# Performance work log

Hardware: AMD Instinct MI355X
Metric: run time of the kernel (lower is better)

## Reference

```python
import jax, jax.numpy as jnp
import numpy as np

# hyperparameters (see init_kwargs)
DP, DS, DO, D, K, C = 256, 256, 64, 320, 10, 10
SI, NS = 100, 22
ALIGN = 0.05
COEF = 0.3989422917366028  # 1/sqrt(2*pi)
B, SEQ, T_STEPS = 32, 512, 200


def _linear_params(key, fan_in, fan_out):
    # torch nn.Linear default init: U(-1/sqrt(fan_in), 1/sqrt(fan_in))
    s = 1.0 / np.sqrt(fan_in)
    kw, kb = jax.random.split(key)
    w = jax.random.uniform(kw, (fan_in, fan_out), minval=-s, maxval=s, dtype=jnp.float32)
    b = jax.random.uniform(kb, (fan_out,), minval=-s, maxval=s, dtype=jnp.float32)
    return w, b


def setup_inputs() -> dict:
    key = jax.random.key(0)
    ks = jax.random.split(key, 8)
    sentence = jax.random.randint(ks[0], (B, SEQ), 0, SI)
    speaker_id = jax.random.randint(ks[1], (B,), 0, NS)
    Lut_P = jax.random.normal(ks[2], (SI, DP), dtype=jnp.float32)
    Lut_S = jax.random.normal(ks[3], (NS, DS), dtype=jnp.float32)
    Na_w, Na_b = _linear_params(ks[4], D * K, 3 * C)
    Nu_w, Nu_b = _linear_params(ks[5], D * K, D)
    No_w, No_b = _linear_params(ks[6], D * K, DO)
    kf = jax.random.split(ks[7], 2)
    Fu_w, Fu_b = _linear_params(kf[0], DS, DP)
    Fo_w, Fo_b = _linear_params(kf[1], DS, D * K)
    return dict(sentence=sentence, speaker_id=speaker_id, Lut_P=Lut_P, Lut_S=Lut_S,
                Na_w=Na_w, Na_b=Na_b, Nu_w=Nu_w, Nu_b=Nu_b, No_w=No_w, No_b=No_b,
                Fu_w=Fu_w, Fu_b=Fu_b, Fo_w=Fo_w, Fo_b=Fo_b, T=T_STEPS)


def reference(sentence, speaker_id, Lut_P, Lut_S, Na_w, Na_b, Nu_w, Nu_b,
              No_w, No_b, Fu_w, Fu_b, Fo_w, Fo_b, T):
    batch, seq_len = sentence.shape
    # Encoder: embedding lookups
    lut_p = Lut_P[sentence]          # (B, S, dp)
    ident = Lut_S[speaker_id]        # (B, ds)

    # ident-dependent terms are loop-invariant; hoist out of the scan
    idt = jnp.tanh(ident @ Fu_w + Fu_b)   # (B, dp)
    fo = ident @ Fo_w + Fo_b              # (B, d*k)

    # initialize(): buffer seeded with speaker embedding in first dp rows
    S0 = jnp.zeros((batch, D, K), dtype=lut_p.dtype)
    S0 = S0.at[:, :DP, :].set(ident[:, :, None])
    mu0 = jnp.zeros((batch, C), dtype=lut_p.dtype)
    o0 = jnp.zeros((batch, DO), dtype=lut_p.dtype)

    J = jnp.arange(1, seq_len + 1, dtype=lut_p.dtype)  # (S,)

    def step(carry, _):
        S_tm1, mu_tm1, o_tm1 = carry
        # --- GMM attention ---
        out = (S_tm1.reshape(batch, D * K) @ Na_w + Na_b).reshape(batch, 3, C)
        k_t, b_t, y_t = out[:, 0], out[:, 1], out[:, 2]
        mu_t = mu_tm1 + ALIGN * jnp.exp(k_t)            # (B, c)
        sig_t = jnp.exp(b_t)                            # (B, c)
        g_t = jax.nn.softmax(y_t, axis=1)               # (B, c)
        # phi: (B, c, S)
        phi = g_t[:, :, None] * jnp.exp(-0.5 * sig_t[:, :, None] * (mu_t[:, :, None] - J) ** 2)
        alpha = COEF * phi.sum(axis=1)                  # (B, S)
        c_t = jnp.einsum('bs,bsd->bd', alpha, lut_p)    # (B, dp)
        # --- Decoder buffer update ---
        C_t = jnp.concatenate([c_t + idt, o_tm1 / 30.0], axis=1)        # (B, d)
        Sp = jnp.concatenate([C_t[:, :, None], S_tm1[:, :, :-1]], axis=2)  # (B, d, k)
        u = Sp.reshape(batch, D * K) @ Nu_w + Nu_b                      # (B, d)
        S_t = jnp.concatenate([u[:, :, None], S_tm1[:, :, :-1]], axis=2)
        o_t = (S_t.reshape(batch, D * K) + fo) @ No_w + No_b            # (B, do)
        return (S_t, mu_t, o_t), o_t

    (_, _, _), outs = jax.lax.scan(step, (S0, mu0, o0), None, length=T)
    return outs  # (T, B, do)
```

## Files before the change

### kernel.cpp

```cpp
#include <hip/hip_runtime.h>

#define DP   256
#define DD   320
#define KK   10
#define CC   10
#define DOUT 64
#define SEQn 512
#define BB   32
#define SI   100
#define NSL  32
#define NGR  8
#define BPG  4
#define NTH  640
#define DPS  10
#define RPS  100

#define CFBASE 1024
#define PSA   448
#define UF_O  0
#define ZA_O  40
#define ZO_O  168
#define HALF_A (NGR*NSL*PSA)
#define PSB   320
#define PUBA_OFF 2048
#define PUBB_OFF (PUBA_OFF + 2*HALF_A)

typedef float f4 __attribute__((ext_vector_type(4)));

__device__ __forceinline__ void llc_ld(f4* dst, const float* p) {
    f4 r;
    asm volatile("global_load_dwordx4 %0, %1, off sc0 sc1" : "=&v"(r) : "v"(p));
    asm volatile("s_waitcnt vmcnt(0)" ::: "memory");
    __builtin_amdgcn_sched_barrier(0);
    *dst = r;
}
__device__ __forceinline__ void llc_st(float* p, f4 v) {
    asm volatile("global_store_dwordx4 %0, %1, off sc0 sc1" :: "v"(p), "v"(v) : "memory");
}

__global__ void prep_kernel(int* ctr) {
    int i = blockIdx.x * blockDim.x + threadIdx.x;
    if (i < 2048) ctr[i] = 0;
}

__device__ __forceinline__ void gbar8(int* base, int slice, int target) {
    asm volatile("s_waitcnt vmcnt(0)" ::: "memory");
    __syncthreads();
    if (threadIdx.x == 0)
        __hip_atomic_fetch_add(&base[(slice & 7) * 16], 1, __ATOMIC_RELEASE, __HIP_MEMORY_SCOPE_AGENT);
    if (threadIdx.x < 8) {
        for (;;) {
            int v = __hip_atomic_load(&base[threadIdx.x * 16], __ATOMIC_RELAXED, __HIP_MEMORY_SCOPE_AGENT);
            v += __shfl_xor(v, 1, 8);
            v += __shfl_xor(v, 2, 8);
            v += __shfl_xor(v, 4, 8);
            if (v >= target) break;
            __builtin_amdgcn_s_sleep(2);
        }
    }
    __syncthreads();
}

__global__ __launch_bounds__(NTH) void recur_kernel(
    const int* __restrict__ sentence, const int* __restrict__ speaker,
    const float* __restrict__ LutP, const float* __restrict__ LutS,
    const float* __restrict__ NaW,  const float* __restrict__ NaB,
    const float* __restrict__ NuW,  const float* __restrict__ NuB,
    const float* __restrict__ NoW,  const float* __restrict__ NoB,
    const float* __restrict__ FuW,  const float* __restrict__ FuB,
    const float* __restrict__ FoW,  const float* __restrict__ FoB,
    float* __restrict__ ws, const int* __restrict__ Tptr,
    float* __restrict__ out)
{
    const int tid  = threadIdx.x;
    const int s    = blockIdx.x & (NSL - 1);
    const int g    = blockIdx.x >> 5;
    const bool owner = (s < BPG);
    const int dbase = s * DPS;
    const int rbase = s * RPS;
    int*  ctr  = (int*)ws + g * 128;
    int*  CFg  = (int*)ws + CFBASE + g * 64;
    float* pubA = ws + PUBA_OFF;
    float* pubB = ws + PUBB_OFF;

    const int c_   = tid >> 6;
    const int lane = tid & 63;

    __shared__ float xsE[BPG][3328];
    __shared__ float wNa[RPS][32];
    __shared__ float wNo[RPS][65];
    __shared__ float naT0[DPS][32];
    __shared__ float noT0[DPS][65];
    __shared__ float identsh[BPG][DP];
    __shared__ float ufull[BPG][DD];
    __shared__ float colL[BPG][DD];
    __shared__ float ucol[BPG*DPS];
    __shared__ float zr[BPG*32];
    __shared__ float zor[BPG*DOUT];
    __shared__ float zastage[NSL][32];
    __shared__ float zostage[NSL][DOUT];
    __shared__ float fos[BPG][RPS];
    __shared__ float nubO[DPS];
    __shared__ float nabL[32];
    __shared__ float aoutL[32];
    __shared__ float muL[CC], sgL[CC], ggL[CC];
    __shared__ float alphaL[SEQn];
    __shared__ float histL[SI];
    __shared__ float idtF[DP];
    __shared__ float colF[DD];
    __shared__ float o_own[DOUT];
    __shared__ float foNoL[DOUT];
    __shared__ int   sentL[SEQn];
    __shared__ int   posidx[SEQn];
    __shared__ int   vstart[SI + 1];
    __shared__ int   vcnt[SI];

    for (int i = tid; i < RPS * 30; i += NTH) {
        int r = i / 30, c = i % 30;
        wNa[r][c] = NaW[(rbase + r) * 30 + c];
    }
    for (int i = tid; i < RPS * 64; i += NTH) {
        int r = i / 64, o = i % 64;
        wNo[r][o] = NoW[(rbase + r) * 64 + o];
    }
    if (tid < DPS * 30) { int dl = tid / 30, c = tid % 30; naT0[dl][c] = NaW[((dbase + dl) * KK) * 30 + c]; }
    if (tid < DPS * 64) { int dl = tid >> 6, o = tid & 63; noT0[dl][o] = NoW[((dbase + dl) * KK) * 64 + o]; }
    if (tid < DPS) nubO[tid] = NuB[dbase + tid];
    if (tid >= 16 && tid < 48) { int c = tid - 16; nabL[c] = (c < 30) ? NaB[c] : 0.f; }
    for (int i = tid; i < BPG * DP; i += NTH) {
        int j = i / DP, v = i % DP;
        identsh[j][v] = LutS[speaker[g * BPG + j] * DP + v];
    }
    __syncthreads();

    float w[50];
    #pragma unroll
    for (int q = 0; q < 50; ++q)
        w[q] = NuW[(size_t)(lane * 50 + q) * DD + dbase + c_];

    for (int i = tid; i < BPG * RPS; i += NTH) {
        int j = i / RPS, r = i % RPS;
        float acc = FoB[rbase + r];
        for (int v = 0; v < DP; v += 8) {
            float wv[8];
            #pragma unroll
            for (int e = 0; e < 8; ++e) wv[e] = FoW[(v + e) * 3200 + rbase + r];
            #pragma unroll
            for (int e = 0; e < 8; ++e) acc += identsh[j][v + e] * wv[e];
        }
        fos[j][r] = acc;
    }
    if (owner) {
        if (tid < DP) {
            float acc = FuB[tid];
            for (int v = 0; v < DP; v += 8) {
                float wv[8];
                #pragma unroll
                for (int e = 0; e < 8; ++e) wv[e] = FuW[(v + e) * DP + tid];
                #pragma unroll
                for (int e = 0; e < 8; ++e) acc += identsh[s][v + e] * wv[e];
            }
            idtF[tid] = tanhf(acc);
        }
        if (tid >= 512 && tid < 512 + CC) muL[tid - 512] = 0.f;
        if (tid < SEQn) sentL[tid] = sentence[(g * BPG + s) * SEQn + tid];
        __syncthreads();
        if (tid < SI) { int cnt = 0; for (int q = 0; q < SEQn; ++q) if (sentL[q] == tid) ++cnt; vcnt[tid] = cnt; }
        __syncthreads();
        if (tid == 0) { int run = 0; for (int v = 0; v < SI; ++v) { vstart[v] = run; run += vcnt[v]; } vstart[SI] = run; }
        __syncthreads();
        if (tid < SI) { int k = vstart[tid]; for (int q = 0; q < SEQn; ++q) if (sentL[q] == tid) posidx[k++] = q; }
    }
    for (int i = tid; i < BPG * 3200; i += NTH) {
        int j = i / 3200, row = i % 3200;
        int d = row / KK;
        xsE[j][(row / 50) * 52 + (row % 50)] = (d < DP) ? identsh[j][d] : 0.f;
    }
    __syncthreads();
    if (tid < 128) {
        int j = tid >> 5, c = tid & 31;
        float acc = 0.f;
        if (c < 30)
            for (int rr = 0; rr < RPS; ++rr) {
                int row = rbase + rr;
                acc += xsE[j][(row / 50) * 52 + (row % 50)] * wNa[rr][c];
            }
        zr[j * 32 + c] = acc;
    }
    if (tid >= 128 && tid < 384) {
        int t = tid - 128, j = t >> 6, o = t & 63;
        float acc = 0.f;
        for (int rr = 0; rr < RPS; ++rr) acc += fos[j][rr] * wNo[rr][o];
        zor[j * 64 + o] = acc;
    }
    __syncthreads();
    {
        float* pa0 = pubA + (size_t)(g * NSL + s) * PSA;
        if (tid < 32) llc_st(pa0 + ZA_O + tid * 4, *(f4*)&zr[tid * 4]);
        if (tid >= 32 && tid < 96) { int q = tid - 32; llc_st(pa0 + ZO_O + q * 4, *(f4*)&zor[q * 4]); }
    }
    gbar8(ctr, s, 32 * 1);

    const int T = Tptr[0];

    for (int i = 0; i < T; ++i) {
        const int rh = i & 1, wh = rh ^ 1;
        float* pa_r = pubA + (size_t)rh * HALF_A + (size_t)g * NSL * PSA;
        float* pa_w = pubA + (size_t)wh * HALF_A + (size_t)(g * NSL + s) * PSA;

        {
            f4 v_uf = {0,0,0,0}, v_za = {0,0,0,0}, v_zo = {0,0,0,0};
            const bool h_uf = (i > 0 && tid < 320);
            const bool h_za = (owner && tid >= 320 && tid < 576);
            const bool h_zo = (owner && tid < 512);
            if (h_uf) {
                const float* p = pa_r + (tid / 10) * PSA + UF_O + (tid % 10) * 4;
                asm volatile("global_load_dwordx4 %0, %1, off sc0 sc1" : "=&v"(v_uf) : "v"(p));
            }
            if (h_za) {
                int t = tid - 320;
                const float* p = pa_r + (t >> 3) * PSA + ZA_O + s * 32 + (t & 7) * 4;
                asm volatile("global_load_dwordx4 %0, %1, off sc0 sc1" : "=&v"(v_za) : "v"(p));
            }
            if (h_zo) {
                const float* p = pa_r + (tid >> 4) * PSA + ZO_O + s * 64 + (tid & 15) * 4;
                asm volatile("global_load_dwordx4 %0, %1, off sc0 sc1" : "=&v"(v_zo) : "v"(p));
            }
            asm volatile("s_waitcnt vmcnt(0)" ::: "memory");
            __builtin_amdgcn_sched_barrier(0);
            if (h_uf) {
                int p = tid / 10, q = tid % 10;
                #pragma unroll
                for (int e = 0; e < 4; ++e) { int f = q * 4 + e; ufull[f / 10][p * 10 + (f % 10)] = v_uf[e]; }
            }
            if (h_za) { int t = tid - 320; *(f4*)&zastage[t >> 3][(t & 7) * 4] = v_za; }
            if (h_zo) { *(f4*)&zostage[tid >> 4][(tid & 15) * 4] = v_zo; }
        }
        __syncthreads();

        if (owner) {
            if (tid < 30) {
                float a = nabL[tid];
                for (int p = 0; p < NSL; ++p) a += zastage[p][tid];
                aoutL[tid] = a;
            }
            if (tid >= 64 && tid < 128) {
                int o = tid - 64;
                float v = 0.f;
                for (int p = 0; p < NSL; ++p) v += zostage[p][o];
                if (i == 0) { foNoL[o] = NoB[o] + v; o_own[o] = 0.f; }
                else        o_own[o] = foNoL[o] + v;
            }
            __syncthreads();
            if (tid < CC) {
                muL[tid] += 0.05f * expf(aoutL[tid]);
                sgL[tid] = expf(aoutL[10 + tid]);
                float m = -1e30f;
                for (int q = 0; q < CC; ++q) m = fmaxf(m, aoutL[20 + q]);
                float ssum = 0.f;
                for (int q = 0; q < CC; ++q) ssum += expf(aoutL[20 + q] - m);
                ggL[tid] = expf(aoutL[20 + tid] - m) / ssum;
            }
            __syncthreads();
            if (tid < SEQn) {
                float J = (float)(tid + 1);
                float a = 0.f;
                #pragma unroll
                for (int c = 0; c < CC; ++c) { float dm = muL[c] - J; a += ggL[c] * __expf(-0.5f * sgL[c] * dm * dm); }
                alphaL[tid] = a * 0.3989422917366028f;
            }
            __syncthreads();
            if (tid < SI) {
                float h = 0.f;
                for (int k = vstart[tid]; k < vstart[tid + 1]; ++k) h += alphaL[posidx[k]];
                histL[tid] = h;
            }
            __syncthreads();
            if (tid < DP) {
                float acc = idtF[tid];
                for (int v = 0; v < SI; v += 10) {
                    float wv[10];
                    #pragma unroll
                    for (int e = 0; e < 10; ++e) wv[e] = LutP[(v + e) * DP + tid];
                    #pragma unroll
                    for (int e = 0; e < 10; ++e) acc += histL[v + e] * wv[e];
                }
                colF[tid] = acc;
            } else if (tid < DD) {
                colF[tid] = o_own[tid - DP] * (1.0f / 30.0f);
            }
            __syncthreads();
            if (tid < 64) {
                float* pb = pubB + (size_t)(g * BPG + s) * PSB;
                for (int q = tid; q < 80; q += 64) llc_st(pb + q * 4, *(f4*)&colF[q * 4]);
                asm volatile("s_waitcnt vmcnt(0)" ::: "memory");
                if (tid == 0)
                    __hip_atomic_store(&CFg[s * 16], i + 1, __ATOMIC_RELEASE, __HIP_MEMORY_SCOPE_AGENT);
            }
            if (i > 0 && tid >= 64 && tid < 128)
                out[((size_t)(i - 1) * BB + (g * BPG + s)) * DOUT + (tid - 64)] = o_own[tid - 64];
        }

        for (int it = tid; it < BPG * DD; it += NTH) {
            int j = it / DD, d = it % DD;
            float* p = &xsE[j][(d / 5) * 52 + (d % 5) * 10];
            float t0 = p[0];
            float v1 = p[1], v2 = p[2], v3 = p[3], v4 = p[4], v5 = p[5], v6 = p[6], v7 = p[7], v8 = p[8];
            p[1] = (i == 0) ? t0 : ufull[j][d];
            p[2] = v1; p[3] = v2; p[4] = v3; p[5] = v4; p[6] = v5; p[7] = v6; p[8] = v7; p[9] = v8;
        }
        if (tid < BPG) {
            while (__hip_atomic_load(&CFg[tid * 16], __ATOMIC_RELAXED, __HIP_MEMORY_SCOPE_AGENT) < i + 1)
                __builtin_amdgcn_s_sleep(2);
        }
        __syncthreads();

        if (tid < 320) {
            int j = tid / 80, q = tid % 80;
            f4 v; llc_ld(&v, pubB + (size_t)(g * BPG + j) * PSB + q * 4);
            #pragma unroll
            for (int e = 0; e < 4; ++e) colL[j][q * 4 + e] = v[e];
        }
        __syncthreads();
        for (int it = tid; it < BPG * DD; it += NTH) {
            int j = it / DD, d = it % DD;
            xsE[j][(d / 5) * 52 + (d % 5) * 10] = colL[j][d];
        }
        __syncthreads();

        {
            float accE[BPG];
            #pragma unroll
            for (int j = 0; j < BPG; ++j) {
                const float* xb = &xsE[j][lane * 52];
                float a = 0.f;
                #pragma unroll
                for (int qq = 0; qq < 12; ++qq) {
                    f4 x = *(const f4*)(xb + qq * 4);
                    a += x.x * w[qq * 4] + x.y * w[qq * 4 + 1] + x.z * w[qq * 4 + 2] + x.w * w[qq * 4 + 3];
                }
                a += xb[48] * w[48] + xb[49] * w[49];
                accE[j] = a;
            }
            #pragma unroll
            for (int j = 0; j < BPG; ++j)
                for (int off = 32; off; off >>= 1) accE[j] += __shfl_xor(accE[j], off, 64);
            if (lane == 0) {
                #pragma unroll
                for (int j = 0; j < BPG; ++j) ucol[j * DPS + c_] = accE[j] + nubO[c_];
            }
        }
        __syncthreads();
        if (tid < 10) llc_st(pa_w + UF_O + tid * 4, *(f4*)&ucol[tid * 4]);

        if (tid < 128) {
            int j = tid >> 5, c = tid & 31;
            float acc = 0.f;
            if (c < 30) {
                for (int dd = 0; dd < DPS; ++dd) {
                    int rg = 2 * s + (dd >= 5);
                    int of = dd * 10 - (dd >= 5 ? 50 : 0);
                    const float* xb = &xsE[j][rg * 52 + of];
                    #pragma unroll
                    for (int k = 1; k < KK; ++k) acc += xb[k] * wNa[dd * 10 + k][c];
                }
                #pragma unroll
                for (int dl = 0; dl < DPS; ++dl) acc += ucol[j * DPS + dl] * naT0[dl][c];
            }
            zr[j * 32 + c] = acc;
        }
        if (tid >= 128 && tid < 384) {
            int t = tid - 128, j = t >> 6, o = t & 63;
            float acc = 0.f;
            for (int dd = 0; dd < DPS; ++dd) {
                int rg = 2 * s + (dd >= 5);
                int of = dd * 10 - (dd >= 5 ? 50 : 0);
                const float* xb = &xsE[j][rg * 52 + of];
                #pragma unroll
                for (int k = 1; k < KK; ++k) acc += xb[k] * wNo[dd * 10 + k][o];
            }
            #pragma unroll
            for (int dl = 0; dl < DPS; ++dl) acc += ucol[j * DPS + dl] * noT0[dl][o];
            zor[j * 64 + o] = acc;
        }
        __syncthreads();

        if (tid >= 10 && tid < 42)  { int q = tid - 10; llc_st(pa_w + ZA_O + q * 4, *(f4*)&zr[q * 4]); }
        if (tid >= 42 && tid < 106) { int q = tid - 42; llc_st(pa_w + ZO_O + q * 4, *(f4*)&zor[q * 4]); }
        gbar8(ctr, s, 32 * (i + 2));
    }

    if (owner) {
        const float* pa_r = pubA + (size_t)(T & 1) * HALF_A + (size_t)g * NSL * PSA;
        if (tid < 512) {
            f4 v; llc_ld(&v, pa_r + (tid >> 4) * PSA + ZO_O + s * 64 + (tid & 15) * 4);
            *(f4*)&zostage[tid >> 4][(tid & 15) * 4] = v;
        }
        __syncthreads();
        if (tid < DOUT) {
            float v = foNoL[tid];
            for (int p = 0; p < NSL; ++p) v += zostage[p][tid];
            out[((size_t)(T - 1) * BB + (g * BPG + s)) * DOUT + tid] = v;
        }
    }
}

extern "C" void kernel_launch(void* const* d_in, const int* in_sizes, int n_in,
                              void* d_out, int out_size, void* d_ws, size_t ws_size,
                              hipStream_t stream) {
    const int*   sentence = (const int*)d_in[0];
    const int*   speaker  = (const int*)d_in[1];
    const float* LutP = (const float*)d_in[2];
    const float* LutS = (const float*)d_in[3];
    const float* NaW  = (const float*)d_in[4];
    const float* NaB  = (const float*)d_in[5];
    const float* NuW  = (const float*)d_in[6];
    const float* NuB  = (const float*)d_in[7];
    const float* NoW  = (const float*)d_in[8];
    const float* NoB  = (const float*)d_in[9];
    const float* FuW  = (const float*)d_in[10];
    const float* FuB  = (const float*)d_in[11];
    const float* FoW  = (const float*)d_in[12];
    const float* FoB  = (const float*)d_in[13];
    const int*   Tptr = (const int*)d_in[14];
    float* ws   = (float*)d_ws;
    float* outp = (float*)d_out;

    hipLaunchKernelGGL(prep_kernel, dim3(2), dim3(1024), 0, stream, (int*)d_ws);
    hipLaunchKernelGGL(recur_kernel, dim3(NSL * NGR), dim3(NTH), 0, stream,
                       sentence, speaker, LutP, LutS, NaW, NaB,
                       NuW, NuB, NoW, NoB, FuW, FuB, FoW, FoB,
                       ws, Tptr, outp);
}
```

Baseline: 4.607 ms.

## Replicate attention/context compute in every block to shrink the per-step broadcast payload

Owner blocks used to compute the attention window, the histogram and the context column for their batch element, then publish a 320-float column to the other 31 slice blocks. Now owners publish only the reduced 96-float pre-activation sums, and every block redundantly computes mu, sigma, softmax, alpha, the histogram and the LutP context for all 4 batch elements itself. This is meant to remove the serial owner-only compute phase from the critical path between the flag release and the other blocks' wait, and to cut the cross-block transfer. The cost is extra redundant ALU and LutP reads in every block each step, plus more shared memory.

```diff
diff --git a/kernel.cpp b/kernel.cpp
--- a/kernel.cpp
+++ b/kernel.cpp
@@ -21,9 +21,8 @@
 #define ZA_O  40
 #define ZO_O  168
 #define HALF_A (NGR*NSL*PSA)
-#define PSB   320
 #define PUBA_OFF 2048
-#define PUBB_OFF (PUBA_OFF + 2*HALF_A)
+#define PUBR_OFF (PUBA_OFF + 2*HALF_A)
 
 typedef float f4 __attribute__((ext_vector_type(4)));
 
@@ -81,7 +80,7 @@
     int*  ctr  = (int*)ws + g * 128;
     int*  CFg  = (int*)ws + CFBASE + g * 64;
     float* pubA = ws + PUBA_OFF;
-    float* pubB = ws + PUBB_OFF;
+    float* pubR = ws + PUBR_OFF;
 
     const int c_   = tid >> 6;
     const int lane = tid & 63;
@@ -102,18 +101,19 @@
     __shared__ float fos[BPG][RPS];
     __shared__ float nubO[DPS];
     __shared__ float nabL[32];
-    __shared__ float aoutL[32];
-    __shared__ float muL[CC], sgL[CC], ggL[CC];
-    __shared__ float alphaL[SEQn];
-    __shared__ float histL[SI];
-    __shared__ float idtF[DP];
-    __shared__ float colF[DD];
-    __shared__ float o_own[DOUT];
-    __shared__ float foNoL[DOUT];
-    __shared__ int   sentL[SEQn];
-    __shared__ int   posidx[SEQn];
-    __shared__ int   vstart[SI + 1];
-    __shared__ int   vcnt[SI];
+    __shared__ float redL[96];
+    __shared__ float red4[BPG][96];
+    __shared__ float aout4[BPG][32];
+    __shared__ float oprev4[BPG][DOUT];
+    __shared__ float foNo4[BPG][DOUT];
+    __shared__ float mu4[BPG][CC], sg4[BPG][CC], gg4[BPG][CC];
+    __shared__ float alpha4[BPG][SEQn];
+    __shared__ float hist4[BPG][104];
+    __shared__ float idtF4[BPG][DP];
+    __shared__ short sentL4[BPG][SEQn];
+    __shared__ short posidx4[BPG][SEQn];
+    __shared__ int   vstart4[BPG][104];
+    __shared__ int   vcnt[104];
 
     for (int i = tid; i < RPS * 30; i += NTH) {
         int r = i / 30, c = i % 30;
@@ -127,10 +127,13 @@
     if (tid < DPS * 64) { int dl = tid >> 6, o = tid & 63; noT0[dl][o] = NoW[((dbase + dl) * KK) * 64 + o]; }
     if (tid < DPS) nubO[tid] = NuB[dbase + tid];
     if (tid >= 16 && tid < 48) { int c = tid - 16; nabL[c] = (c < 30) ? NaB[c] : 0.f; }
+    if (tid >= 64 && tid < 104) mu4[(tid - 64) / 10][(tid - 64) % 10] = 0.f;
     for (int i = tid; i < BPG * DP; i += NTH) {
         int j = i / DP, v = i % DP;
         identsh[j][v] = LutS[speaker[g * BPG + j] * DP + v];
     }
+    for (int i = tid; i < BPG * SEQn; i += NTH)
+        sentL4[i / SEQn][i % SEQn] = (short)sentence[(g * BPG + i / SEQn) * SEQn + i % SEQn];
     __syncthreads();
 
     float w[50];
@@ -150,26 +153,26 @@
         }
         fos[j][r] = acc;
     }
-    if (owner) {
-        if (tid < DP) {
-            float acc = FuB[tid];
-            for (int v = 0; v < DP; v += 8) {
-                float wv[8];
-                #pragma unroll
-                for (int e = 0; e < 8; ++e) wv[e] = FuW[(v + e) * DP + tid];
-                #pragma unroll
-                for (int e = 0; e < 8; ++e) acc += identsh[s][v + e] * wv[e];
-            }
-            idtF[tid] = tanhf(acc);
-        }
-        if (tid >= 512 && tid < 512 + CC) muL[tid - 512] = 0.f;
-        if (tid < SEQn) sentL[tid] = sentence[(g * BPG + s) * SEQn + tid];
-        __syncthreads();
-        if (tid < SI) { int cnt = 0; for (int q = 0; q < SEQn; ++q) if (sentL[q] == tid) ++cnt; vcnt[tid] = cnt; }
-        __syncthreads();
-        if (tid == 0) { int run = 0; for (int v = 0; v < SI; ++v) { vstart[v] = run; run += vcnt[v]; } vstart[SI] = run; }
-        __syncthreads();
-        if (tid < SI) { int k = vstart[tid]; for (int q = 0; q < SEQn; ++q) if (sentL[q] == tid) posidx[k++] = q; }
+    for (int idx = tid; idx < BPG * DP; idx += NTH) {
+        int j = idx / DP, d = idx % DP;
+        float acc = FuB[d];
+        for (int v = 0; v < DP; v += 8) {
+            float wv[8];
+            #pragma unroll
+            for (int e = 0; e < 8; ++e) wv[e] = FuW[(v + e) * DP + d];
+            #pragma unroll
+            for (int e = 0; e < 8; ++e) acc += identsh[j][v + e] * wv[e];
+        }
+        idtF4[j][d] = tanhf(acc);
+    }
+    __syncthreads();
+    for (int j = 0; j < BPG; ++j) {
+        if (tid < SI) { int cnt = 0; for (int q = 0; q < SEQn; ++q) cnt += (sentL4[j][q] == tid); vcnt[tid] = cnt; }
+        __syncthreads();
+        if (tid == 0) { int run = 0; for (int v = 0; v < SI; ++v) { vstart4[j][v] = run; run += vcnt[v]; } vstart4[j][SI] = run; }
+        __syncthreads();
+        if (tid < SI) { int k = vstart4[j][tid]; for (int q = 0; q < SEQn; ++q) if (sentL4[j][q] == tid) posidx4[j][k++] = (short)q; }
+        __syncthreads();
     }
     for (int i = tid; i < BPG * 3200; i += NTH) {
         int j = i / 3200, row = i % 3200;
@@ -240,65 +243,24 @@
 
         if (owner) {
             if (tid < 30) {
-                float a = nabL[tid];
+                float a = 0.f;
                 for (int p = 0; p < NSL; ++p) a += zastage[p][tid];
-                aoutL[tid] = a;
+                redL[tid] = a;
             }
             if (tid >= 64 && tid < 128) {
                 int o = tid - 64;
                 float v = 0.f;
                 for (int p = 0; p < NSL; ++p) v += zostage[p][o];
-                if (i == 0) { foNoL[o] = NoB[o] + v; o_own[o] = 0.f; }
-                else        o_own[o] = foNoL[o] + v;
-            }
-            __syncthreads();
-            if (tid < CC) {
-                muL[tid] += 0.05f * expf(aoutL[tid]);
-                sgL[tid] = expf(aoutL[10 + tid]);
-                float m = -1e30f;
-                for (int q = 0; q < CC; ++q) m = fmaxf(m, aoutL[20 + q]);
-                float ssum = 0.f;
-                for (int q = 0; q < CC; ++q) ssum += expf(aoutL[20 + q] - m);
-                ggL[tid] = expf(aoutL[20 + tid] - m) / ssum;
-            }
-            __syncthreads();
-            if (tid < SEQn) {
-                float J = (float)(tid + 1);
-                float a = 0.f;
-                #pragma unroll
-                for (int c = 0; c < CC; ++c) { float dm = muL[c] - J; a += ggL[c] * __expf(-0.5f * sgL[c] * dm * dm); }
-                alphaL[tid] = a * 0.3989422917366028f;
-            }
-            __syncthreads();
-            if (tid < SI) {
-                float h = 0.f;
-                for (int k = vstart[tid]; k < vstart[tid + 1]; ++k) h += alphaL[posidx[k]];
-                histL[tid] = h;
-            }
-            __syncthreads();
-            if (tid < DP) {
-                float acc = idtF[tid];
-                for (int v = 0; v < SI; v += 10) {
-                    float wv[10];
-                    #pragma unroll
-                    for (int e = 0; e < 10; ++e) wv[e] = LutP[(v + e) * DP + tid];
-                    #pragma unroll
-                    for (int e = 0; e < 10; ++e) acc += histL[v + e] * wv[e];
-                }
-                colF[tid] = acc;
-            } else if (tid < DD) {
-                colF[tid] = o_own[tid - DP] * (1.0f / 30.0f);
+                redL[32 + o] = v;
             }
             __syncthreads();
             if (tid < 64) {
-                float* pb = pubB + (size_t)(g * BPG + s) * PSB;
-                for (int q = tid; q < 80; q += 64) llc_st(pb + q * 4, *(f4*)&colF[q * 4]);
+                float* pr = pubR + (size_t)(g * BPG + s) * 128;
+                if (tid < 24) llc_st(pr + tid * 4, *(f4*)&redL[tid * 4]);
                 asm volatile("s_waitcnt vmcnt(0)" ::: "memory");
                 if (tid == 0)
                     __hip_atomic_store(&CFg[s * 16], i + 1, __ATOMIC_RELEASE, __HIP_MEMORY_SCOPE_AGENT);
             }
-            if (i > 0 && tid >= 64 && tid < 128)
-                out[((size_t)(i - 1) * BB + (g * BPG + s)) * DOUT + (tid - 64)] = o_own[tid - 64];
         }
 
         for (int it = tid; it < BPG * DD; it += NTH) {
@@ -314,12 +276,73 @@
                 __builtin_amdgcn_s_sleep(2);
         }
         __syncthreads();
-
-        if (tid < 320) {
-            int j = tid / 80, q = tid % 80;
-            f4 v; llc_ld(&v, pubB + (size_t)(g * BPG + j) * PSB + q * 4);
-            #pragma unroll
-            for (int e = 0; e < 4; ++e) colL[j][q * 4 + e] = v[e];
+        if (tid < 96) {
+            int j = tid / 24, q = tid % 24;
+            f4 v; llc_ld(&v, pubR + (size_t)(g * BPG + j) * 128 + q * 4);
+            *(f4*)&red4[j][q * 4] = v;
+        }
+        __syncthreads();
+        if (tid < 120) {
+            int j = tid / 30, c = tid % 30;
+            aout4[j][c] = nabL[c] + red4[j][c];
+        } else if (tid >= 128 && tid < 384) {
+            int t = tid - 128, j = t >> 6, o = t & 63;
+            float v = red4[j][32 + o];
+            if (i == 0) { foNo4[j][o] = NoB[o] + v; oprev4[j][o] = 0.f; }
+            else        oprev4[j][o] = foNo4[j][o] + v;
+        }
+        __syncthreads();
+        if (i > 0 && s < BPG && tid >= 64 && tid < 128)
+            out[((size_t)(i - 1) * BB + (g * BPG + s)) * DOUT + (tid - 64)] = oprev4[s][tid - 64];
+
+        if (tid < 40) {
+            int j = tid / 10, c = tid % 10;
+            mu4[j][c] += 0.05f * expf(aout4[j][c]);
+            sg4[j][c] = expf(aout4[j][10 + c]);
+            float m = -1e30f;
+            for (int q = 0; q < CC; ++q) m = fmaxf(m, aout4[j][20 + q]);
+            float ss = 0.f;
+            for (int q = 0; q < CC; ++q) ss += expf(aout4[j][20 + q] - m);
+            gg4[j][c] = expf(aout4[j][20 + c] - m) / ss;
+        }
+        __syncthreads();
+        if (tid < SEQn) {
+            float J = (float)(tid + 1);
+            #pragma unroll
+            for (int j = 0; j < BPG; ++j) {
+                float a = 0.f;
+                #pragma unroll
+                for (int c = 0; c < CC; ++c) { float dm = mu4[j][c] - J; a += gg4[j][c] * __expf(-0.5f * sg4[j][c] * dm * dm); }
+                alpha4[j][tid] = a * 0.3989422917366028f;
+            }
+        }
+        __syncthreads();
+        if (tid < 400) {
+            int j = tid / 100, v = tid % 100;
+            float h = 0.f;
+            for (int k = vstart4[j][v]; k < vstart4[j][v + 1]; ++k) h += alpha4[j][posidx4[j][k]];
+            hist4[j][v] = h;
+        }
+        __syncthreads();
+        if (tid < DP) {
+            float a0 = idtF4[0][tid], a1 = idtF4[1][tid], a2 = idtF4[2][tid], a3 = idtF4[3][tid];
+            for (int v = 0; v < SI; v += 10) {
+                float wv[10];
+                #pragma unroll
+                for (int e = 0; e < 10; ++e) wv[e] = LutP[(v + e) * DP + tid];
+                #pragma unroll
+                for (int e = 0; e < 10; ++e) {
+                    a0 += hist4[0][v + e] * wv[e];
+                    a1 += hist4[1][v + e] * wv[e];
+                    a2 += hist4[2][v + e] * wv[e];
+                    a3 += hist4[3][v + e] * wv[e];
+                }
+            }
+            colL[0][tid] = a0; colL[1][tid] = a1; colL[2][tid] = a2; colL[3][tid] = a3;
+        } else if (tid < DP + DOUT) {
+            int o = tid - DP;
+            #pragma unroll
+            for (int j = 0; j < BPG; ++j) colL[j][DP + o] = oprev4[j][o] * (1.0f / 30.0f);
         }
         __syncthreads();
         for (int it = tid; it < BPG * DD; it += NTH) {
@@ -398,7 +421,7 @@
         }
         __syncthreads();
         if (tid < DOUT) {
-            float v = foNoL[tid];
+            float v = foNo4[s][tid];
             for (int p = 0; p < NSL; ++p) v += zostage[p][tid];
             out[((size_t)(T - 1) * BB + (g * BPG + s)) * DOUT + tid] = v;
         }
```

Measured after the change: 8.671 ms. +88.2%, slower.
